# Kernel optimization log

Hardware: AMD Instinct MI355X
Metric: run time of the kernel (lower is better)

## Reference

```python
import jax, jax.numpy as jnp
import numpy as np
import math

D_MODEL = 1024
N_HEADS = 16
HEAD_DIM = D_MODEL // N_HEADS
B, T = 4, 2048


def setup_inputs() -> dict:
    key = jax.random.key(0)
    k1, k2, k3, k4, k5 = jax.random.split(key, 5)
    s = 1.0 / math.sqrt(D_MODEL)
    return {
        "x": jax.random.normal(k1, (B, T, D_MODEL), dtype=jnp.float32),
        "qkv_w": jax.random.normal(k2, (3 * D_MODEL, D_MODEL), dtype=jnp.float32) * s,
        "qkv_b": jax.random.normal(k3, (3 * D_MODEL,), dtype=jnp.float32) * 0.02,
        "out_w": jax.random.normal(k4, (D_MODEL, D_MODEL), dtype=jnp.float32) * s,
        "out_b": jax.random.normal(k5, (D_MODEL,), dtype=jnp.float32) * 0.02,
    }


def reference(x, qkv_w, qkv_b, out_w, out_b) -> jnp.ndarray:
    b, t, c = x.shape
    h, hd = N_HEADS, HEAD_DIM
    # qkv projection: [B,T,3C]
    qkv = jnp.einsum("btc,oc->bto", x, qkv_w) + qkv_b
    qkv = qkv.reshape(b, t, 3, h, hd).transpose(2, 0, 3, 1, 4)  # [3,B,H,T,hd]
    q, k, v = qkv[0], qkv[1], qkv[2]
    scale = 1.0 / math.sqrt(hd)
    attn = jnp.einsum("bhqd,bhkd->bhqk", q, k) * scale  # [B,H,T,T]
    causal = jnp.triu(jnp.ones((t, t), dtype=bool), k=1)
    attn = jnp.where(causal, -jnp.inf, attn)
    attn = jax.nn.softmax(attn, axis=-1)
    out = jnp.einsum("bhqk,bhkd->bhqd", attn, v)  # [B,H,T,hd]
    out = out.transpose(0, 2, 1, 3).reshape(b, t, c)
    return jnp.einsum("btc,oc->bto", out, out_w) + out_b
```

## Files before the change

### kernel.cpp

```cpp
#include <hip/hip_runtime.h>
#include <stdint.h>
#include <stddef.h>

#define TT 2048
#define NH 16
#define HD 64
#define CM 1024
#define QSCALE 0.1803368801f
#define PPAD 72

typedef float f32x4  __attribute__((ext_vector_type(4)));
typedef short bf16x8 __attribute__((ext_vector_type(8)));

static __device__ __forceinline__ unsigned short f32_to_bf16(float f) {
    union { float f; unsigned u; } c; c.f = f;
    unsigned u = c.u;
    u += 0x7FFFu + ((u >> 16) & 1u);
    return (unsigned short)(u >> 16);
}

static __device__ __forceinline__ unsigned pack_bf16_trunc(float lo, float hi) {
    return __builtin_amdgcn_perm(__float_as_uint(hi), __float_as_uint(lo), 0x07060302u);
}

static __device__ __forceinline__ void glds16(const unsigned short* g, unsigned short* l) {
    __builtin_amdgcn_global_load_lds(
        (const __attribute__((address_space(1))) unsigned int*)g,
        (__attribute__((address_space(3))) unsigned int*)l,
        16, 0, 0);
}

static __device__ __forceinline__ void drain_glds_then_barrier() {
    asm volatile("s_waitcnt vmcnt(0)" ::: "memory");
    __syncthreads();
}

__global__ __launch_bounds__(256) void cast_all(
    const float* __restrict__ x, const float* __restrict__ w1,
    const float* __restrict__ w2,
    unsigned short* __restrict__ X16, unsigned short* __restrict__ W1o,
    unsigned short* __restrict__ W2o) {
    int i = blockIdx.x * blockDim.x + threadIdx.x;
    const float* src; unsigned short* dst; int j;
    if (i < 2097152)      { src = x;  dst = X16; j = i; }
    else if (i < 2883584) { src = w1; dst = W1o; j = i - 2097152; }
    else                  { src = w2; dst = W2o; j = i - 2883584; }
    float4 v = ((const float4*)src)[j];
    ushort4 o;
    o.x = f32_to_bf16(v.x); o.y = f32_to_bf16(v.y);
    o.z = f32_to_bf16(v.z); o.w = f32_to_bf16(v.w);
    ((ushort4*)dst)[j] = o;
}

__device__ __forceinline__ void gemm_core_128x128(
    const unsigned short* __restrict__ A,
    const unsigned short* __restrict__ Bm,
    int K, int m0, int n0,
    unsigned short* ldsA, unsigned short* ldsB,
    f32x4 acc[4][4])
{
    const int tid  = threadIdx.x;
    const int lane = tid & 63;
    const int wm   = ((tid >> 6) >> 1) * 64;
    const int wn   = ((tid >> 6) & 1) * 64;
    const int l15  = lane & 15;
    const int quad = lane >> 4;

    const int c1 = tid, c2 = tid + 256;
    const unsigned short* gA1 = A  + (size_t)(m0 + (c1 >> 2)) * K + (c1 & 3) * 8;
    const unsigned short* gA2 = A  + (size_t)(m0 + (c2 >> 2)) * K + (c2 & 3) * 8;
    const unsigned short* gB1 = Bm + (size_t)(n0 + (c1 >> 2)) * K + (c1 & 3) * 8;
    const unsigned short* gB2 = Bm + (size_t)(n0 + (c2 >> 2)) * K + (c2 & 3) * 8;
    unsigned short* dA1 = ldsA + (c1 & ~63) * 8;
    unsigned short* dA2 = ldsA + (c2 & ~63) * 8;
    unsigned short* dB1 = ldsB + (c1 & ~63) * 8;
    unsigned short* dB2 = ldsB + (c2 & ~63) * 8;

    for (int k0 = 0; k0 < K; k0 += 32) {
        glds16(gA1 + k0, dA1);
        glds16(gA2 + k0, dA2);
        glds16(gB1 + k0, dB1);
        glds16(gB2 + k0, dB2);
        drain_glds_then_barrier();

        bf16x8 af[4], bfr[4];
        #pragma unroll
        for (int mi = 0; mi < 4; ++mi)
            af[mi] = *(const bf16x8*)(ldsA + (wm + mi * 16 + l15) * 32 + quad * 8);
        #pragma unroll
        for (int ni = 0; ni < 4; ++ni)
            bfr[ni] = *(const bf16x8*)(ldsB + (wn + ni * 16 + l15) * 32 + quad * 8);

        #pragma unroll
        for (int mi = 0; mi < 4; ++mi)
            #pragma unroll
            for (int ni = 0; ni < 4; ++ni)
                acc[mi][ni] = __builtin_amdgcn_mfma_f32_16x16x32_bf16(
                    af[mi], bfr[ni], acc[mi][ni], 0, 0, 0);
        __syncthreads();
    }
}

__global__ __launch_bounds__(256) void gemm_qkv(
    const unsigned short* __restrict__ X,
    const unsigned short* __restrict__ W,
    const float* __restrict__ bias,
    unsigned short* __restrict__ Qb,
    unsigned short* __restrict__ Kb,
    unsigned short* __restrict__ Vt)
{
    __shared__ __align__(16) unsigned short lds[8704];
    unsigned short* ldsA = lds;
    unsigned short* ldsB = lds + 4096;
    const int m0 = blockIdx.y * 128;
    const int n0 = blockIdx.x * 128;

    f32x4 acc[4][4];
    f32x4 z = {0.f, 0.f, 0.f, 0.f};
    #pragma unroll
    for (int mi = 0; mi < 4; ++mi)
        #pragma unroll
        for (int ni = 0; ni < 4; ++ni) acc[mi][ni] = z;

    gemm_core_128x128(X, W, CM, m0, n0, ldsA, ldsB, acc);

    const int tid  = threadIdx.x;
    const int lane = tid & 63;
    const int w    = tid >> 6;
    const int wm   = (w >> 1) * 64;
    const int wn   = (w & 1) * 64;
    const int l15  = lane & 15;
    const int quad = lane >> 4;
    const int region = n0 >> 10;
    const int b_idx = m0 >> 11;
    const int t0 = m0 & 2047;

    if (region == 2) {
        #pragma unroll
        for (int half = 0; half < 2; ++half) {
            if ((w & 1) == half) {
                #pragma unroll
                for (int ni = 0; ni < 4; ++ni) {
                    const int orow = ni * 16 + l15;
                    const float bv = bias[n0 + half * 64 + orow];
                    #pragma unroll
                    for (int mi = 0; mi < 4; ++mi) {
                        uint2 pk;
                        pk.x = (unsigned)f32_to_bf16(acc[mi][ni][0] + bv) |
                               ((unsigned)f32_to_bf16(acc[mi][ni][1] + bv) << 16);
                        pk.y = (unsigned)f32_to_bf16(acc[mi][ni][2] + bv) |
                               ((unsigned)f32_to_bf16(acc[mi][ni][3] + bv) << 16);
                        *(uint2*)(lds + orow * 136 + wm + mi * 16 + quad * 4) = pk;
                    }
                }
            }
            __syncthreads();
            {
                const int row = tid >> 2, seg = tid & 3;
                const int o   = n0 + half * 64 + row;
                const int oin = o & 1023;
                const int hh  = oin >> 6, d = oin & 63;
                unsigned short* dst = Vt + ((size_t)((b_idx << 4) + hh) * HD + d) * TT
                                        + t0 + seg * 32;
                const unsigned short* src = lds + row * 136 + seg * 32;
                #pragma unroll
                for (int u = 0; u < 4; ++u)
                    *(uint4*)(dst + u * 8) = *(const uint4*)(src + u * 8);
            }
            __syncthreads();
        }
        return;
    }

    #pragma unroll
    for (int ni = 0; ni < 4; ++ni) {
        const int o   = n0 + wn + ni * 16 + l15;
        const float bv = bias[o];
        const int oin = o & 1023;
        const int h = oin >> 6, d = oin & 63;
        #pragma unroll
        for (int mi = 0; mi < 4; ++mi) {
            #pragma unroll
            for (int r = 0; r < 4; ++r) {
                const int gm = m0 + wm + mi * 16 + quad * 4 + r;
                const int b  = gm >> 11, t = gm & 2047;
                const float val = acc[mi][ni][r] + bv;
                const int bh = (b << 4) + h;
                if (region == 0)
                    Qb[(((size_t)bh * TT + t) << 6) + d] = f32_to_bf16(val * QSCALE);
                else
                    Kb[(((size_t)bh * TT + t) << 6) + d] = f32_to_bf16(val);
            }
        }
    }
}

__global__ __launch_bounds__(256, 2) void attn_kernel(
    const unsigned short* __restrict__ Qb,
    const unsigned short* __restrict__ Kb,
    const unsigned short* __restrict__ Vt,
    unsigned short* __restrict__ CTX)
{
    __shared__ __align__(16) unsigned short Kl[2][64 * 64];
    __shared__ __align__(16) unsigned short Vl[2][64 * 64];
    __shared__ __align__(16) unsigned short Pl[8][16 * PPAD];

    const int pair = blockIdx.x;
    const int h = blockIdx.y, b = blockIdx.z;
    const int tid  = threadIdx.x;
    const int lane = tid & 63;
    const int w    = tid >> 6;
    const int l15  = lane & 15;
    const int quad = lane >> 4;
    const int sw   = l15 & 7;
    const int bh   = b * NH + h;

    const unsigned short* Kbase = Kb + (size_t)bh * TT * HD;
    const unsigned short* Vbase = Vt + (size_t)bh * HD * TT;
    const f32x4 z = {0.f, 0.f, 0.f, 0.f};

    const int c1 = tid, c2 = tid + 256;
    const int row1 = c1 >> 3, col1 = ((c1 & 7) ^ (row1 & 7)) * 8;
    const int row2 = c2 >> 3, col2 = ((c2 & 7) ^ (row2 & 7)) * 8;
    unsigned short* dK1 = &Kl[0][(c1 & ~63) * 8];
    unsigned short* dK2 = &Kl[0][(c2 & ~63) * 8];
    unsigned short* dV1 = &Vl[0][(c1 & ~63) * 8];
    unsigned short* dV2 = &Vl[0][(c2 & ~63) * 8];

    for (int j = 0; j < 2; ++j) {
        const int qt = j ? pair : 15 - pair;
        const int kt_last = 2 * qt + 1;
        const int qb0 = qt * 128;

        const unsigned short* kp1 = Kbase + (size_t)row1 * HD + col1;
        const unsigned short* kp2 = Kbase + (size_t)row2 * HD + col2;
        const unsigned short* vp1 = Vbase + (size_t)row1 * TT + col1;
        const unsigned short* vp2 = Vbase + (size_t)row2 * TT + col2;

        bf16x8 qf[2][2];
        #pragma unroll
        for (int f = 0; f < 2; ++f) {
            const unsigned short* qr =
                Qb + (size_t)(bh * TT + qb0 + f * 64 + w * 16 + l15) * HD + quad * 8;
            qf[f][0] = *(const bf16x8*)(qr);
            qf[f][1] = *(const bf16x8*)(qr + 32);
        }

        f32x4 o_acc[2][4];
        #pragma unroll
        for (int f = 0; f < 2; ++f)
            #pragma unroll
            for (int di = 0; di < 4; ++di) o_acc[f][di] = z;
        float lrun[2] = {0.f, 0.f};

        __syncthreads();
        glds16(kp1, dK1); glds16(kp2, dK2);
        glds16(vp1, dV1); glds16(vp2, dV2);
        kp1 += 64 * HD; kp2 += 64 * HD; vp1 += 64; vp2 += 64;

        for (int kt = 0; kt <= kt_last; ++kt) {
            const int cur = kt & 1;
            drain_glds_then_barrier();
            if (kt < kt_last) {
                const int nx = (cur ^ 1) * 4096;
                glds16(kp1, dK1 + nx); glds16(kp2, dK2 + nx);
                glds16(vp1, dV1 + nx); glds16(vp2, dV2 + nx);
                kp1 += 64 * HD; kp2 += 64 * HD; vp1 += 64; vp2 += 64;
            }

            const unsigned short* Kt = Kl[cur];
            const unsigned short* Vtile = Vl[cur];
            const bool f0act = (kt < kt_last);

            f32x4 s0[4], s1[4];
            #pragma unroll
            for (int ni = 0; ni < 4; ++ni) {
                const unsigned short* kr = Kt + (ni * 16 + l15) * 64;
                bf16x8 kf0 = *(const bf16x8*)(kr + ((quad ^ sw) * 8));
                bf16x8 kf1 = *(const bf16x8*)(kr + (((quad + 4) ^ sw) * 8));
                if (f0act) {
                    f32x4 a = __builtin_amdgcn_mfma_f32_16x16x32_bf16(kf0, qf[0][0], z, 0, 0, 0);
                    s0[ni] = __builtin_amdgcn_mfma_f32_16x16x32_bf16(kf1, qf[0][1], a, 0, 0, 0);
                }
                f32x4 a1 = __builtin_amdgcn_mfma_f32_16x16x32_bf16(kf0, qf[1][0], z, 0, 0, 0);
                s1[ni] = __builtin_amdgcn_mfma_f32_16x16x32_bf16(kf1, qf[1][1], a1, 0, 0, 0);
            }

            const int qloc = w * 16 + l15;
            if (f0act && kt == 2 * qt) {
                #pragma unroll
                for (int ni = 0; ni < 4; ++ni)
                    #pragma unroll
                    for (int r = 0; r < 4; ++r)
                        if (ni * 16 + quad * 4 + r > qloc) s0[ni][r] = -1e30f;
            }
            if (kt == kt_last) {
                #pragma unroll
                for (int ni = 0; ni < 4; ++ni)
                    #pragma unroll
                    for (int r = 0; r < 4; ++r)
                        if (ni * 16 + quad * 4 + r > qloc) s1[ni][r] = -1e30f;
            }

            #define SOFTMAX_P(S, F)                                              \
            {                                                                    \
                float acc_l = 0.f;                                               \
                _Pragma("unroll")                                                \
                for (int ni = 0; ni < 4; ++ni)                                   \
                    _Pragma("unroll")                                            \
                    for (int r = 0; r < 4; ++r) {                                \
                        float p = __builtin_amdgcn_exp2f(S[ni][r]);              \
                        S[ni][r] = p;                                            \
                        acc_l += p;                                              \
                    }                                                            \
                lrun[F] += acc_l;                                                \
                unsigned short* pwf = Pl[w * 2 + F];                             \
                _Pragma("unroll")                                                \
                for (int ni = 0; ni < 4; ++ni) {                                 \
                    uint2 pk;                                                    \
                    pk.x = pack_bf16_trunc(S[ni][0], S[ni][1]);                  \
                    pk.y = pack_bf16_trunc(S[ni][2], S[ni][3]);                  \
                    *(uint2*)(pwf + l15 * PPAD + ni * 16 + quad * 4) = pk;       \
                }                                                                \
            }

            if (f0act) SOFTMAX_P(s0, 0);
            SOFTMAX_P(s1, 1);
            #undef SOFTMAX_P

            asm volatile("s_waitcnt lgkmcnt(0)" ::: "memory");

            const unsigned short* pw0 = Pl[w * 2 + 0];
            const unsigned short* pw1 = Pl[w * 2 + 1];
            if (f0act) {
                #pragma unroll
                for (int c = 0; c < 2; ++c) {
                    bf16x8 pf0 = *(const bf16x8*)(pw0 + l15 * PPAD + c * 32 + quad * 8);
                    bf16x8 pf1 = *(const bf16x8*)(pw1 + l15 * PPAD + c * 32 + quad * 8);
                    #pragma unroll
                    for (int di = 0; di < 4; ++di) {
                        const unsigned short* vr = Vtile + (di * 16 + l15) * 64
                                                 + (((c * 4 + quad) ^ sw) * 8);
                        bf16x8 vf = *(const bf16x8*)(vr);
                        o_acc[0][di] = __builtin_amdgcn_mfma_f32_16x16x32_bf16(vf, pf0, o_acc[0][di], 0, 0, 0);
                        o_acc[1][di] = __builtin_amdgcn_mfma_f32_16x16x32_bf16(vf, pf1, o_acc[1][di], 0, 0, 0);
                    }
                }
            } else {
                #pragma unroll
                for (int c = 0; c < 2; ++c) {
                    bf16x8 pf1 = *(const bf16x8*)(pw1 + l15 * PPAD + c * 32 + quad * 8);
                    #pragma unroll
                    for (int di = 0; di < 4; ++di) {
                        const unsigned short* vr = Vtile + (di * 16 + l15) * 64
                                                 + (((c * 4 + quad) ^ sw) * 8);
                        bf16x8 vf = *(const bf16x8*)(vr);
                        o_acc[1][di] = __builtin_amdgcn_mfma_f32_16x16x32_bf16(vf, pf1, o_acc[1][di], 0, 0, 0);
                    }
                }
            }
        }

        #pragma unroll
        for (int f = 0; f < 2; ++f) {
            float lt = lrun[f];
            lt += __shfl_xor(lt, 16);
            lt += __shfl_xor(lt, 32);
            const float inv = 1.0f / lt;
            unsigned short* crow =
                CTX + (size_t)(b * TT + qb0 + f * 64 + w * 16 + l15) * CM + h * HD;
            #pragma unroll
            for (int di = 0; di < 4; ++di) {
                uint2 pk;
                pk.x = (unsigned)f32_to_bf16(o_acc[f][di][0] * inv) |
                       ((unsigned)f32_to_bf16(o_acc[f][di][1] * inv) << 16);
                pk.y = (unsigned)f32_to_bf16(o_acc[f][di][2] * inv) |
                       ((unsigned)f32_to_bf16(o_acc[f][di][3] * inv) << 16);
                *(uint2*)(crow + di * 16 + quad * 4) = pk;
            }
        }
    }
}

__global__ __launch_bounds__(256) void gemm_out(
    const unsigned short* __restrict__ CTX,
    const unsigned short* __restrict__ W,
    const float* __restrict__ bias,
    float* __restrict__ out)
{
    __shared__ __align__(16) unsigned short ldsA[128 * 32];
    __shared__ __align__(16) unsigned short ldsB[128 * 32];
    const int m0 = blockIdx.y * 128;
    const int n0 = blockIdx.x * 128;

    f32x4 acc[4][4];
    f32x4 z = {0.f, 0.f, 0.f, 0.f};
    #pragma unroll
    for (int mi = 0; mi < 4; ++mi)
        #pragma unroll
        for (int ni = 0; ni < 4; ++ni) acc[mi][ni] = z;

    gemm_core_128x128(CTX, W, CM, m0, n0, ldsA, ldsB, acc);

    const int tid  = threadIdx.x;
    const int lane = tid & 63;
    const int w    = tid >> 6;
    const int wm   = (w >> 1) * 64;
    const int wn   = (w & 1) * 64;
    const int l15  = lane & 15;
    const int quad = lane >> 4;

    #pragma unroll
    for (int ni = 0; ni < 4; ++ni) {
        const int o = n0 + wn + ni * 16 + l15;
        const float bv = bias[o];
        #pragma unroll
        for (int mi = 0; mi < 4; ++mi) {
            #pragma unroll
            for (int r = 0; r < 4; ++r) {
                const int gm = m0 + wm + mi * 16 + quad * 4 + r;
                out[(size_t)gm * CM + o] = acc[mi][ni][r] + bv;
            }
        }
    }
}

extern "C" void kernel_launch(void* const* d_in, const int* in_sizes, int n_in,
                              void* d_out, int out_size, void* d_ws, size_t ws_size,
                              hipStream_t stream) {
    const float* x     = (const float*)d_in[0];
    const float* qkv_w = (const float*)d_in[1];
    const float* qkv_b = (const float*)d_in[2];
    const float* out_w = (const float*)d_in[3];
    const float* out_b = (const float*)d_in[4];
    float* out = (float*)d_out;

    char* ws = (char*)d_ws;
    unsigned short* X16 = (unsigned short*)(ws + 0);
    unsigned short* W1  = (unsigned short*)(ws + 16777216);
    unsigned short* W2  = (unsigned short*)(ws + 23068672);
    unsigned short* Qb  = (unsigned short*)(ws + 25165824);
    unsigned short* Kb  = (unsigned short*)(ws + 41943040);
    unsigned short* Vt  = (unsigned short*)(ws + 58720256);
    unsigned short* CTX = (unsigned short*)(ws + 75497472);

    cast_all<<<12288, 256, 0, stream>>>(x, qkv_w, out_w, X16, W1, W2);

    gemm_qkv<<<dim3(24, 64), 256, 0, stream>>>(X16, W1, qkv_b, Qb, Kb, Vt);
    attn_kernel<<<dim3(8, NH, 4), 256, 0, stream>>>(Qb, Kb, Vt, CTX);
    gemm_out<<<dim3(8, 64), 256, 0, stream>>>(CTX, W2, out_b, out);
}
```

Before: 273.3 us.

## Double-buffer GEMM LDS tiles and swap MFMA operands for vectorized epilogue stores

The shared GEMM core now double-buffers the A/B LDS tiles, issuing the next k-slice's global-to-LDS loads before computing the current one. This is meant to hide load latency behind MFMA work and drops one barrier per iteration. For the Q/K projection and the output GEMM, the MFMA operands are swapped so each lane holds four consecutive output columns. That lets the epilogues write packed bf16x4 or float4 stores and load the bias as a float4 instead of doing scalar scattered stores. It also doubles LDS usage and adds launch_bounds occupancy hints plus a stronger waitcnt in the barrier.

```diff
diff --git a/kernel.cpp b/kernel.cpp
--- a/kernel.cpp
+++ b/kernel.cpp
@@ -30,8 +30,8 @@
         16, 0, 0);
 }
 
-static __device__ __forceinline__ void drain_glds_then_barrier() {
-    asm volatile("s_waitcnt vmcnt(0)" ::: "memory");
+static __device__ __forceinline__ void hard_barrier() {
+    asm volatile("s_waitcnt vmcnt(0) lgkmcnt(0)" ::: "memory");
     __syncthreads();
 }
 
@@ -52,11 +52,12 @@
     ((ushort4*)dst)[j] = o;
 }
 
-__device__ __forceinline__ void gemm_core_128x128(
+template<bool SWAP>
+__device__ __forceinline__ void gemm_core_dbuf(
     const unsigned short* __restrict__ A,
     const unsigned short* __restrict__ Bm,
     int K, int m0, int n0,
-    unsigned short* ldsA, unsigned short* ldsB,
+    unsigned short* lds,
     f32x4 acc[4][4])
 {
     const int tid  = threadIdx.x;
@@ -65,6 +66,9 @@
     const int wn   = ((tid >> 6) & 1) * 64;
     const int l15  = lane & 15;
     const int quad = lane >> 4;
+
+    unsigned short* ldsA = lds;
+    unsigned short* ldsB = lds + 8192;
 
     const int c1 = tid, c2 = tid + 256;
     const unsigned short* gA1 = A  + (size_t)(m0 + (c1 >> 2)) * K + (c1 & 3) * 8;
@@ -76,32 +80,41 @@
     unsigned short* dB1 = ldsB + (c1 & ~63) * 8;
     unsigned short* dB2 = ldsB + (c2 & ~63) * 8;
 
-    for (int k0 = 0; k0 < K; k0 += 32) {
-        glds16(gA1 + k0, dA1);
-        glds16(gA2 + k0, dA2);
-        glds16(gB1 + k0, dB1);
-        glds16(gB2 + k0, dB2);
-        drain_glds_then_barrier();
+    glds16(gA1, dA1); glds16(gA2, dA2);
+    glds16(gB1, dB1); glds16(gB2, dB2);
+    gA1 += 32; gA2 += 32; gB1 += 32; gB2 += 32;
+
+    int step = 0;
+    for (int k0 = 0; k0 < K; k0 += 32, step ^= 1) {
+        hard_barrier();
+        if (k0 + 32 < K) {
+            const int nx = (step ^ 1) * 4096;
+            glds16(gA1, dA1 + nx); glds16(gA2, dA2 + nx);
+            glds16(gB1, dB1 + nx); glds16(gB2, dB2 + nx);
+            gA1 += 32; gA2 += 32; gB1 += 32; gB2 += 32;
+        }
+        const unsigned short* tA = ldsA + step * 4096;
+        const unsigned short* tB = ldsB + step * 4096;
 
         bf16x8 af[4], bfr[4];
         #pragma unroll
         for (int mi = 0; mi < 4; ++mi)
-            af[mi] = *(const bf16x8*)(ldsA + (wm + mi * 16 + l15) * 32 + quad * 8);
+            af[mi] = *(const bf16x8*)(tA + (wm + mi * 16 + l15) * 32 + quad * 8);
         #pragma unroll
         for (int ni = 0; ni < 4; ++ni)
-            bfr[ni] = *(const bf16x8*)(ldsB + (wn + ni * 16 + l15) * 32 + quad * 8);
+            bfr[ni] = *(const bf16x8*)(tB + (wn + ni * 16 + l15) * 32 + quad * 8);
 
         #pragma unroll
         for (int mi = 0; mi < 4; ++mi)
             #pragma unroll
             for (int ni = 0; ni < 4; ++ni)
-                acc[mi][ni] = __builtin_amdgcn_mfma_f32_16x16x32_bf16(
-                    af[mi], bfr[ni], acc[mi][ni], 0, 0, 0);
-        __syncthreads();
+                acc[mi][ni] = SWAP
+                    ? __builtin_amdgcn_mfma_f32_16x16x32_bf16(bfr[ni], af[mi], acc[mi][ni], 0, 0, 0)
+                    : __builtin_amdgcn_mfma_f32_16x16x32_bf16(af[mi], bfr[ni], acc[mi][ni], 0, 0, 0);
     }
 }
 
-__global__ __launch_bounds__(256) void gemm_qkv(
+__global__ __launch_bounds__(256, 2) void gemm_qkv(
     const unsigned short* __restrict__ X,
     const unsigned short* __restrict__ W,
     const float* __restrict__ bias,
@@ -109,9 +122,7 @@
     unsigned short* __restrict__ Kb,
     unsigned short* __restrict__ Vt)
 {
-    __shared__ __align__(16) unsigned short lds[8704];
-    unsigned short* ldsA = lds;
-    unsigned short* ldsB = lds + 4096;
+    __shared__ __align__(16) unsigned short lds[16384];
     const int m0 = blockIdx.y * 128;
     const int n0 = blockIdx.x * 128;
 
@@ -122,7 +133,9 @@
         #pragma unroll
         for (int ni = 0; ni < 4; ++ni) acc[mi][ni] = z;
 
-    gemm_core_128x128(X, W, CM, m0, n0, ldsA, ldsB, acc);
+    const bool qk = (n0 < 2048);
+    if (qk) gemm_core_dbuf<true >(X, W, CM, m0, n0, lds, acc);
+    else    gemm_core_dbuf<false>(X, W, CM, m0, n0, lds, acc);
 
     const int tid  = threadIdx.x;
     const int lane = tid & 63;
@@ -131,11 +144,11 @@
     const int wn   = (w & 1) * 64;
     const int l15  = lane & 15;
     const int quad = lane >> 4;
-    const int region = n0 >> 10;
     const int b_idx = m0 >> 11;
     const int t0 = m0 & 2047;
 
-    if (region == 2) {
+    if (!qk) {
+        hard_barrier();
         #pragma unroll
         for (int half = 0; half < 2; ++half) {
             if ((w & 1) == half) {
@@ -154,7 +167,7 @@
                     }
                 }
             }
-            __syncthreads();
+            hard_barrier();
             {
                 const int row = tid >> 2, seg = tid & 3;
                 const int o   = n0 + half * 64 + row;
@@ -167,30 +180,33 @@
                 for (int u = 0; u < 4; ++u)
                     *(uint4*)(dst + u * 8) = *(const uint4*)(src + u * 8);
             }
-            __syncthreads();
+            hard_barrier();
         }
         return;
     }
 
+    const int region = n0 >> 10;
+    unsigned short* dst0 = region ? Kb : Qb;
+    const float scl = region ? 1.0f : QSCALE;
     #pragma unroll
-    for (int ni = 0; ni < 4; ++ni) {
-        const int o   = n0 + wn + ni * 16 + l15;
-        const float bv = bias[o];
-        const int oin = o & 1023;
-        const int h = oin >> 6, d = oin & 63;
-        #pragma unroll
-        for (int mi = 0; mi < 4; ++mi) {
-            #pragma unroll
-            for (int r = 0; r < 4; ++r) {
-                const int gm = m0 + wm + mi * 16 + quad * 4 + r;
-                const int b  = gm >> 11, t = gm & 2047;
-                const float val = acc[mi][ni][r] + bv;
-                const int bh = (b << 4) + h;
-                if (region == 0)
-                    Qb[(((size_t)bh * TT + t) << 6) + d] = f32_to_bf16(val * QSCALE);
-                else
-                    Kb[(((size_t)bh * TT + t) << 6) + d] = f32_to_bf16(val);
-            }
+    for (int mi = 0; mi < 4; ++mi) {
+        const int gm = m0 + wm + mi * 16 + l15;
+        const int b  = gm >> 11, t = gm & 2047;
+        #pragma unroll
+        for (int ni = 0; ni < 4; ++ni) {
+            const int o  = n0 + wn + ni * 16 + quad * 4;
+            const float4 bv = *(const float4*)(bias + o);
+            const int oin = o & 1023;
+            const int hh = oin >> 6, d = oin & 63;
+            const int bh = (b << 4) + hh;
+            const float v0 = (acc[mi][ni][0] + bv.x) * scl;
+            const float v1 = (acc[mi][ni][1] + bv.y) * scl;
+            const float v2 = (acc[mi][ni][2] + bv.z) * scl;
+            const float v3 = (acc[mi][ni][3] + bv.w) * scl;
+            uint2 pk;
+            pk.x = (unsigned)f32_to_bf16(v0) | ((unsigned)f32_to_bf16(v1) << 16);
+            pk.y = (unsigned)f32_to_bf16(v2) | ((unsigned)f32_to_bf16(v3) << 16);
+            *(uint2*)(dst0 + (((size_t)(bh * TT + t)) << 6) + d) = pk;
         }
     }
 }
@@ -253,14 +269,14 @@
             for (int di = 0; di < 4; ++di) o_acc[f][di] = z;
         float lrun[2] = {0.f, 0.f};
 
-        __syncthreads();
+        hard_barrier();
         glds16(kp1, dK1); glds16(kp2, dK2);
         glds16(vp1, dV1); glds16(vp2, dV2);
         kp1 += 64 * HD; kp2 += 64 * HD; vp1 += 64; vp2 += 64;
 
         for (int kt = 0; kt <= kt_last; ++kt) {
             const int cur = kt & 1;
-            drain_glds_then_barrier();
+            hard_barrier();
             if (kt < kt_last) {
                 const int nx = (cur ^ 1) * 4096;
                 glds16(kp1, dK1 + nx); glds16(kp2, dK2 + nx);
@@ -382,14 +398,13 @@
     }
 }
 
-__global__ __launch_bounds__(256) void gemm_out(
+__global__ __launch_bounds__(256, 2) void gemm_out(
     const unsigned short* __restrict__ CTX,
     const unsigned short* __restrict__ W,
     const float* __restrict__ bias,
     float* __restrict__ out)
 {
-    __shared__ __align__(16) unsigned short ldsA[128 * 32];
-    __shared__ __align__(16) unsigned short ldsB[128 * 32];
+    __shared__ __align__(16) unsigned short lds[16384];
     const int m0 = blockIdx.y * 128;
     const int n0 = blockIdx.x * 128;
 
@@ -400,7 +415,7 @@
         #pragma unroll
         for (int ni = 0; ni < 4; ++ni) acc[mi][ni] = z;
 
-    gemm_core_128x128(CTX, W, CM, m0, n0, ldsA, ldsB, acc);
+    gemm_core_dbuf<true>(CTX, W, CM, m0, n0, lds, acc);
 
     const int tid  = threadIdx.x;
     const int lane = tid & 63;
@@ -411,16 +426,19 @@
     const int quad = lane >> 4;
 
     #pragma unroll
-    for (int ni = 0; ni < 4; ++ni) {
-        const int o = n0 + wn + ni * 16 + l15;
-        const float bv = bias[o];
-        #pragma unroll
-        for (int mi = 0; mi < 4; ++mi) {
-            #pragma unroll
-            for (int r = 0; r < 4; ++r) {
-                const int gm = m0 + wm + mi * 16 + quad * 4 + r;
-                out[(size_t)gm * CM + o] = acc[mi][ni][r] + bv;
-            }
+    for (int mi = 0; mi < 4; ++mi) {
+        const int gm = m0 + wm + mi * 16 + l15;
+        float* orow = out + (size_t)gm * CM;
+        #pragma unroll
+        for (int ni = 0; ni < 4; ++ni) {
+            const int o = n0 + wn + ni * 16 + quad * 4;
+            const float4 bv = *(const float4*)(bias + o);
+            float4 v;
+            v.x = acc[mi][ni][0] + bv.x;
+            v.y = acc[mi][ni][1] + bv.y;
+            v.z = acc[mi][ni][2] + bv.z;
+            v.w = acc[mi][ni][3] + bv.w;
+            *(float4*)(orow + o) = v;
         }
     }
 }
```

After: 262.5 us. 1.04x faster.
